# Kernel tuning notes

Measured on AMD Instinct MI355X. Metric: run time of the kernel, lower is better.

Reference implementation:

```python
import jax, jax.numpy as jnp
import numpy as np

B, S, D = 2, 2048, 1024
H, HD = 16, 64
HIDDEN = 2730  # int(1024 * 4 * 2/3)
WINDOW = 512
EPS = 1e-6


def rmsnorm(x, w):
    return x * jax.lax.rsqrt(jnp.mean(x * x, axis=-1, keepdims=True) + EPS) * w


def rope(q, k):
    # q, k: [B, H, S, HD]; half-split rotate_half convention, base 10000
    inv_freq = 1.0 / (10000.0 ** (jnp.arange(0, HD, 2, dtype=jnp.float32) / HD))
    pos = jnp.arange(S, dtype=jnp.float32)
    freqs = pos[:, None] * inv_freq[None, :]          # [S, HD/2]
    cos = jnp.concatenate([jnp.cos(freqs)] * 2, -1)    # [S, HD]
    sin = jnp.concatenate([jnp.sin(freqs)] * 2, -1)

    def rot_half(x):
        x1, x2 = jnp.split(x, 2, axis=-1)
        return jnp.concatenate([-x2, x1], axis=-1)

    q = q * cos + rot_half(q) * sin
    k = k * cos + rot_half(k) * sin
    return q, k


def setup_inputs() -> dict:
    key = jax.random.key(0)
    ks = jax.random.split(key, 6)
    return {
        "x": jax.random.normal(ks[0], (B, S, D), jnp.float32),
        "norm1_w": jnp.ones((D,), jnp.float32),
        "norm2_w": jnp.ones((D,), jnp.float32),
        "w_qkv": jax.random.normal(ks[1], (3 * D, D), jnp.float32) * 0.02,
        "qnorm_w": jnp.ones((HD,), jnp.float32),
        "knorm_w": jnp.ones((HD,), jnp.float32),
        "w_o": jax.random.normal(ks[2], (D, D), jnp.float32) * (0.02 / 2 ** 0.5),
        "w1": jax.random.normal(ks[3], (HIDDEN, D), jnp.float32) * 0.02,
        "w3": jax.random.normal(ks[4], (HIDDEN, D), jnp.float32) * 0.02,
        "w2": jax.random.normal(ks[5], (D, HIDDEN), jnp.float32) * 0.02,
    }


def reference(x, norm1_w, norm2_w, w_qkv, qnorm_w, knorm_w, w_o, w1, w3, w2):
    h = rmsnorm(x, norm1_w)                              # [B,S,D]
    qkv = jnp.einsum("bsd,ed->bse", h, w_qkv)            # [B,S,3D]
    q, k, v = jnp.split(qkv, 3, axis=-1)

    def heads(t):  # [B,S,D] -> [B,H,S,HD]
        return t.reshape(B, S, H, HD).transpose(0, 2, 1, 3)

    q, k, v = heads(q), heads(k), heads(v)
    q = rmsnorm(q, qnorm_w)  # qk_norm over head_dim
    k = rmsnorm(k, knorm_w)
    q, k = rope(q, k)

    scale = HD ** -0.5
    scores = jnp.einsum("bhqd,bhkd->bhqk", q, k) * scale  # [B,H,S,S]
    pos = jnp.arange(S)
    row, col = pos[:, None], pos[None, :]
    masked = (col > row) | (col < row - WINDOW + 1)       # True = don't attend
    scores = jnp.where(masked[None, None], -jnp.inf, scores)
    attn = jax.nn.softmax(scores, axis=-1)
    out = jnp.einsum("bhqk,bhkd->bhqd", attn, v)          # [B,H,S,HD]
    out = out.transpose(0, 2, 1, 3).reshape(B, S, D)
    out = jnp.einsum("bsd,ed->bse", out, w_o)

    x = x + out
    h2 = rmsnorm(x, norm2_w)
    gate = jax.nn.silu(jnp.einsum("bsd,hd->bsh", h2, w1))
    up = jnp.einsum("bsd,hd->bsh", h2, w3)
    ffn = jnp.einsum("bsh,dh->bsd", gate * up, w2)
    return x + ffn
```

## Files before the change

kernel.cpp:

```cpp
#include <hip/hip_runtime.h>

typedef unsigned short u16;
typedef unsigned int   u32;
typedef __bf16 bf16x8 __attribute__((ext_vector_type(8)));
typedef __bf16 bf16x2 __attribute__((ext_vector_type(2)));
typedef float  f32x4  __attribute__((ext_vector_type(4)));
typedef float  f32x2  __attribute__((ext_vector_type(2)));

#define DEV static __device__ __forceinline__
#define NEG_INF (-__builtin_inff())

DEV u16 f2bf(float f) {
  u32 u = __builtin_bit_cast(u32, f);
  u += 0x7fffu + ((u >> 16) & 1u);
  return (u16)(u >> 16);
}

DEV float bf2f(u16 v) {
  u32 u = (u32)v << 16;
  return __builtin_bit_cast(float, u);
}

DEV u32 packbf(float a, float b) {
  f32x2 v = {a, b};
  bf16x2 r = __builtin_convertvector(v, bf16x2);
  return __builtin_bit_cast(u32, r);
}

typedef __attribute__((address_space(1))) void gvoid_t;
typedef __attribute__((address_space(3))) void svoid_t;

DEV void async16(const void* g, void* l) {
  __builtin_amdgcn_global_load_lds((gvoid_t*)g, (svoid_t*)l, 16, 0, 0);
}

DEV f32x4 mfma_bf16(bf16x8 a, bf16x8 b, f32x4 c) {
  return __builtin_amdgcn_mfma_f32_16x16x32_bf16(a, b, c, 0, 0, 0);
}

#define SBAR() __builtin_amdgcn_sched_barrier(0)
#define BARRIER() do { SBAR(); __builtin_amdgcn_s_barrier(); SBAR(); } while (0)
#define LGK0() do { asm volatile("s_waitcnt lgkmcnt(0)" ::: "memory"); SBAR(); } while (0)
#define VMC(n) do { asm volatile("s_waitcnt vmcnt(" #n ")" ::: "memory"); SBAR(); } while (0)

__global__ void cvt_bf16_k(const float* __restrict__ s, u16* __restrict__ d, int n4) {
  int i = blockIdx.x * blockDim.x + threadIdx.x;
  if (i >= n4) return;
  float4 v = ((const float4*)s)[i];
  ((ushort4*)d)[i] = make_ushort4(f2bf(v.x), f2bf(v.y), f2bf(v.z), f2bf(v.w));
}

__global__ void w13_prep_k(const float* __restrict__ w1, const float* __restrict__ w3,
                           u16* __restrict__ d, int n4) {
  int i = blockIdx.x * blockDim.x + threadIdx.x;
  if (i >= n4) return;
  int e = i * 4;
  int r = e >> 10;
  int c = e & 1023;
  int blk = r >> 4, j = r & 15;
  int srow = (blk >> 1) * 16 + j;
  ushort4 o = make_ushort4(0, 0, 0, 0);
  if (srow < 2730) {
    const float* src = (blk & 1) ? w3 : w1;
    float4 v = *(const float4*)&src[(size_t)srow * 1024 + c];
    o = make_ushort4(f2bf(v.x), f2bf(v.y), f2bf(v.z), f2bf(v.w));
  }
  ((ushort4*)d)[i] = o;
}

__global__ void pad_cols_k(const float* __restrict__ s, u16* __restrict__ d,
                           int Cs, int Cd, int n4) {
  int i = blockIdx.x * blockDim.x + threadIdx.x;
  if (i >= n4) return;
  int e = i * 4;
  int r = e / Cd;
  int c = e - r * Cd;
  u16 o[4];
#pragma unroll
  for (int j = 0; j < 4; ++j) {
    int cc = c + j;
    o[j] = (cc < Cs) ? f2bf(s[(size_t)r * Cs + cc]) : (u16)0;
  }
  ((ushort4*)d)[i] = make_ushort4(o[0], o[1], o[2], o[3]);
}

__global__ void rmsnorm_cvt_k(const float* __restrict__ in, const float* __restrict__ w,
                              u16* __restrict__ out) {
  __shared__ float red[4];
  int row = blockIdx.x;
  int t = threadIdx.x;
  const float4 v = ((const float4*)(in + (size_t)row * 1024))[t];
  float ss = v.x * v.x + v.y * v.y + v.z * v.z + v.w * v.w;
#pragma unroll
  for (int off = 1; off < 64; off <<= 1) ss += __shfl_xor(ss, off);
  if ((t & 63) == 0) red[t >> 6] = ss;
  __syncthreads();
  float tot = red[0] + red[1] + red[2] + red[3];
  float rs = rsqrtf(tot * (1.0f / 1024.0f) + 1e-6f);
  const float4 wv = ((const float4*)w)[t];
  ((ushort4*)(out + (size_t)row * 1024))[t] =
      make_ushort4(f2bf(v.x * rs * wv.x), f2bf(v.y * rs * wv.y),
                   f2bf(v.z * rs * wv.z), f2bf(v.w * rs * wv.w));
}

__global__ void qk_post_k(const u16* __restrict__ qkv, const float* __restrict__ qw,
                          const float* __restrict__ kw, u16* __restrict__ Qb,
                          u16* __restrict__ Kb) {
  int g = blockIdx.x * 4 + (threadIdx.x >> 6);
  int d = threadIdx.x & 63;
  int b = g >> 15;
  int r = g & 32767;
  int s = r >> 4;
  int h = r & 15;
  size_t base = ((size_t)(b * 2048 + s)) * 3072 + h * 64 + d;
  float qv = bf2f(qkv[base]);
  float kv = bf2f(qkv[base + 1024]);
  float q2 = qv * qv, k2 = kv * kv;
#pragma unroll
  for (int off = 1; off < 64; off <<= 1) {
    q2 += __shfl_xor(q2, off);
    k2 += __shfl_xor(k2, off);
  }
  float qn = qv * rsqrtf(q2 * (1.0f / 64.0f) + 1e-6f) * qw[d];
  float kn = kv * rsqrtf(k2 * (1.0f / 64.0f) + 1e-6f) * kw[d];
  int j = d & 31;
  float invf = __expf((float)j * -0.28782313662425572f);
  float ang = (float)s * invf;
  float sn, cs;
  sincosf(ang, &sn, &cs);
  float pq = __shfl_xor(qn, 32);
  float pk = __shfl_xor(kn, 32);
  float qo = (d < 32) ? (qn * cs - pq * sn) : (qn * cs + pq * sn);
  float ko = (d < 32) ? (kn * cs - pk * sn) : (kn * cs + pk * sn);
  size_t ob = ((size_t)((b * 16 + h) * 2048 + s)) * 64 + d;
  Qb[ob] = f2bf(qo);
  Kb[ob] = f2bf(ko);
}

__global__ void vtrans_k(const u16* __restrict__ qkv, u16* __restrict__ VT) {
  __shared__ u16 tile[64][65];
  int bh = blockIdx.y;
  int b = bh >> 4, h = bh & 15;
  int s0 = blockIdx.x * 64;
  int t = threadIdx.x;
  int tx = t & 63, ty = t >> 6;
#pragma unroll
  for (int p = 0; p < 16; ++p) {
    int sl = p * 4 + ty;
    tile[sl][tx] = qkv[((size_t)(b * 2048 + s0 + sl)) * 3072 + 2048 + h * 64 + tx];
  }
  __syncthreads();
#pragma unroll
  for (int p = 0; p < 16; ++p) {
    int dl = p * 4 + ty;
    VT[((size_t)(bh * 64 + dl)) * 2048 + s0 + tx] = tile[tx][dl];
  }
}

template <int EPI>
__global__ __launch_bounds__(256, 1) void gemm128p(
    const u16* __restrict__ A, const u16* __restrict__ B0,
    const float* __restrict__ res, void* __restrict__ outp, int M, int N, int K, int NT) {
  __shared__ u16 S[49152];
  const int tid = threadIdx.x;
  const int lane = tid & 63;
  const int wv = tid >> 6;
  const int wr = wv >> 1;
  const int wc = wv & 1;
  const int c16 = lane & 15, g4 = lane >> 4;

  const int gx = gridDim.x;
  const int nwg = gx * gridDim.y;
  const int lin = blockIdx.x + gx * blockIdx.y;
  const int swz = (lin & 7) * (nwg >> 3) + (lin >> 3);
  const int bm = (swz / gx) * 128;
  const int bn = (swz % gx) * 128;

  const int strow = tid >> 3;
  const int stcs = ((tid & 7) ^ (strow & 7)) * 8;
  const u16* Ap = A + (size_t)(bm + strow) * K + stcs;
  const u16* Bp = B0 + (size_t)(bn + strow) * K + stcs;
  const int wvb = wv * 512;

#define STG(bufi, t) do { const size_t _o = (size_t)(t) * 64; _Pragma("unroll") \
    for (int s = 0; s < 4; ++s) { \
      async16(Ap + _o + (size_t)s * 32 * K, &S[(bufi) * 16384 + s * 2048 + wvb]); \
      async16(Bp + _o + (size_t)s * 32 * K, &S[(bufi) * 16384 + 8192 + s * 2048 + wvb]); \
    } } while (0)

  f32x4 acc[4][4] = {};
  const int xk0 = (g4 ^ (c16 & 7)) * 8;
  const int xk1 = ((4 + g4) ^ (c16 & 7)) * 8;
  const int arb = (wr * 64 + c16) * 64;
  const int brb = 8192 + (wc * 64 + c16) * 64;

  STG(0, 0);
  STG(1, 1);
  VMC(8); BARRIER();

  int cur = 0;
  for (int kt = 0; kt < NT; ++kt) {
    int n2 = cur + 2; if (n2 >= 3) n2 -= 3;
    if (kt + 2 < NT) {
      if (n2 == 0) STG(0, kt + 2);
      else if (n2 == 1) STG(1, kt + 2);
      else STG(2, kt + 2);
    }
    bf16x8 a[4][2], b[4][2];
    const int cb = cur * 16384;
#pragma unroll
    for (int mf = 0; mf < 4; ++mf) {
      a[mf][0] = *(const bf16x8*)&S[cb + arb + mf * 1024 + xk0];
      a[mf][1] = *(const bf16x8*)&S[cb + arb + mf * 1024 + xk1];
    }
#pragma unroll
    for (int nf = 0; nf < 4; ++nf) {
      b[nf][0] = *(const bf16x8*)&S[cb + brb + nf * 1024 + xk0];
      b[nf][1] = *(const bf16x8*)&S[cb + brb + nf * 1024 + xk1];
    }
    LGK0();
    __builtin_amdgcn_s_setprio(1);
#pragma unroll
    for (int ks = 0; ks < 2; ++ks)
#pragma unroll
      for (int mf = 0; mf < 4; ++mf)
#pragma unroll
        for (int nf = 0; nf < 4; ++nf)
          acc[mf][nf] = mfma_bf16(a[mf][ks], b[nf][ks], acc[mf][nf]);
    __builtin_amdgcn_s_setprio(0);
    if (kt + 2 < NT) { VMC(8); } else { VMC(0); }
    BARRIER();
    cur = cur + 1; if (cur >= 3) cur = 0;
  }

#pragma unroll
  for (int mf = 0; mf < 4; ++mf)
#pragma unroll
    for (int nf = 0; nf < 4; ++nf) {
      int row = bm + wr * 64 + mf * 16 + g4 * 4;
      int col = bn + wc * 64 + nf * 16 + c16;
#pragma unroll
      for (int r = 0; r < 4; ++r) {
        size_t idx = (size_t)(row + r) * (size_t)N + col;
        if constexpr (EPI == 1) {
          ((float*)outp)[idx] = res[idx] + acc[mf][nf][r];
        } else {
          ((u16*)outp)[idx] = f2bf(acc[mf][nf][r]);
        }
      }
    }
#undef STG
}

__global__ __launch_bounds__(512, 1) void gemm192(
    const u16* __restrict__ A, const u16* __restrict__ B0,
    u16* __restrict__ outp, int N, int K, int NT) {
  __shared__ u16 SA[32768];
  __shared__ u16 SB[24576];
  const int tid = threadIdx.x;
  const int lane = tid & 63;
  const int wv = tid >> 6;
  const int wr = wv >> 2;
  const int wc = wv & 3;
  const int c16 = lane & 15, g4 = lane >> 4;

  const int gx = gridDim.x;
  const int nwg = gx * gridDim.y;
  const int lin = blockIdx.x + gx * blockIdx.y;
  const int swz = (lin & 7) * (nwg >> 3) + (lin >> 3);
  const int bm = (swz / gx) * 256;
  const int bn = (swz % gx) * 192;

  const int sr = tid >> 2;
  const int sc2s = ((tid & 3) * 16) ^ (((sr >> 3) & 1) << 5);
  const int scol = sc2s >> 1;
  const u16* Asrc = A + (size_t)(bm + sr) * K + scol;
  const int ldst = wv * 512;
  const int brow = tid >> 3;
  const int bgr = (tid & 7) ^ (brow & 7);
  const u16* Bsrc = B0 + (size_t)(bn + brow) * K + bgr * 8;
  const int bldst = wv * 512;

#define STA_(buf, h, t) do { \
    const u16* _g = Asrc + (size_t)(h) * 128 * K + (t) * 64; \
    async16(_g,      &SA[(buf) * 16384 + (h) * 8192 + ldst]); \
    async16(_g + 32, &SA[(buf) * 16384 + (h) * 8192 + 4096 + ldst]); } while (0)
#define STB_(buf, p, t) do { \
    async16(Bsrc + (size_t)(p) * 64 * K + (t) * 64, \
            &SB[(buf) * 12288 + (p) * 4096 + bldst]); } while (0)

  const int xr = (g4 * 8) ^ (((c16 >> 3) & 1) << 4);
  const int raOff = c16 * 32 + xr;
  const int abase0 = wr * 8192;
  const int brow0 = wc * 48 + c16;
  const int bsw = c16 & 7;

#define LDA_(buf, qm) do { _Pragma("unroll") \
    for (int mf = 0; mf < 4; ++mf) { \
      int _ro = (buf) * 16384 + abase0 + ((qm) * 64 + mf * 16) * 32 + raOff; \
      a[mf][0] = *(const bf16x8*)&SA[_ro]; \
      a[mf][1] = *(const bf16x8*)&SA[_ro + 4096]; } } while (0)
#define LDB01_(buf) do { _Pragma("unroll") \
    for (int nf = 0; nf < 2; ++nf) { \
      int _r = (buf) * 12288 + (brow0 + nf * 16) * 64; \
      bq01[nf][0] = *(const bf16x8*)&SB[_r + ((g4) ^ bsw) * 8]; \
      bq01[nf][1] = *(const bf16x8*)&SB[_r + ((4 + g4) ^ bsw) * 8]; } } while (0)
#define LDB2_(buf) do { \
      int _r = (buf) * 12288 + (brow0 + 32) * 64; \
      bq2[0] = *(const bf16x8*)&SB[_r + ((g4) ^ bsw) * 8]; \
      bq2[1] = *(const bf16x8*)&SB[_r + ((4 + g4) ^ bsw) * 8]; } while (0)
#define MM16(qm) do { _Pragma("unroll") \
    for (int mf = 0; mf < 4; ++mf) _Pragma("unroll") \
      for (int nf = 0; nf < 2; ++nf) { \
        acc[(qm) * 4 + mf][nf] = mfma_bf16(a[mf][0], bq01[nf][0], acc[(qm) * 4 + mf][nf]); \
        acc[(qm) * 4 + mf][nf] = mfma_bf16(a[mf][1], bq01[nf][1], acc[(qm) * 4 + mf][nf]); } } while (0)
#define MM8(qm) do { _Pragma("unroll") \
    for (int mf = 0; mf < 4; ++mf) { \
      acc[(qm) * 4 + mf][2] = mfma_bf16(a[mf][0], bq2[0], acc[(qm) * 4 + mf][2]); \
      acc[(qm) * 4 + mf][2] = mfma_bf16(a[mf][1], bq2[1], acc[(qm) * 4 + mf][2]); } } while (0)

  f32x4 acc[8][3] = {};
  bf16x8 a[4][2], bq01[2][2], bq2[2];

  STB_(0, 0, 0); STB_(0, 1, 0); STB_(0, 2, 0); STA_(0, 0, 0); STA_(0, 1, 0);
  STB_(1, 0, 1); STB_(1, 1, 1); STB_(1, 2, 1); STA_(1, 0, 1); STA_(1, 1, 1);
  VMC(7); BARRIER();

  for (int kt = 0; kt < NT; ++kt) {
    const int buf = kt & 1;
    const int t2 = (kt + 2 < NT) ? kt + 2 : NT - 1;
    LDA_(buf, 0); LDB01_(buf);
    BARRIER(); LGK0();
    __builtin_amdgcn_s_setprio(1); MM16(0); __builtin_amdgcn_s_setprio(0);
    BARRIER();
    LDB2_(buf);
    BARRIER(); LGK0();
    __builtin_amdgcn_s_setprio(1); MM8(0); __builtin_amdgcn_s_setprio(0);
    BARRIER();
    LDA_(buf, 1);
    STB_(buf, 0, t2); STB_(buf, 1, t2); STB_(buf, 2, t2);
    BARRIER(); LGK0();
    __builtin_amdgcn_s_setprio(1); MM16(1); __builtin_amdgcn_s_setprio(0);
    BARRIER();
    STA_(buf, 0, t2); STA_(buf, 1, t2);
    BARRIER();
    __builtin_amdgcn_s_setprio(1); MM8(1); __builtin_amdgcn_s_setprio(0);
    VMC(7); BARRIER();
  }
  asm volatile("s_waitcnt vmcnt(0)" ::: "memory");

#pragma unroll
  for (int mf = 0; mf < 8; ++mf) {
    int row0 = bm + wr * 128 + mf * 16 + g4 * 4;
#pragma unroll
    for (int nf = 0; nf < 3; ++nf) {
      int col = bn + wc * 48 + nf * 16 + c16;
#pragma unroll
      for (int r = 0; r < 4; ++r)
        outp[(size_t)(row0 + r) * N + col] = f2bf(acc[mf][nf][r]);
    }
  }
#undef STA_
#undef STB_
#undef LDA_
#undef LDB01_
#undef LDB2_
#undef MM16
#undef MM8
}

template <int QM, int QN>
DEV void mmq(f32x4 (&acc)[8][4], const bf16x8 (&a)[4][2], const bf16x8 (&b)[2][2]) {
#pragma unroll
  for (int mf = 0; mf < 4; ++mf)
#pragma unroll
    for (int nf = 0; nf < 2; ++nf) {
      acc[QM * 4 + mf][QN * 2 + nf] = mfma_bf16(a[mf][0], b[nf][0], acc[QM * 4 + mf][QN * 2 + nf]);
      acc[QM * 4 + mf][QN * 2 + nf] = mfma_bf16(a[mf][1], b[nf][1], acc[QM * 4 + mf][QN * 2 + nf]);
    }
}

template <int EPI>
__global__ __launch_bounds__(512, 2) void gemm256(
    const u16* __restrict__ A, const u16* __restrict__ B0,
    void* __restrict__ outp, int M, int N, int K, int NT) {
  __shared__ u16 S[65536];
  const int tid = threadIdx.x;
  const int lane = tid & 63;
  const int wv = tid >> 6;
  const int wr = wv >> 2;
  const int wc = wv & 3;
  const int c16 = lane & 15, g4 = lane >> 4;

  int gx = gridDim.x;
  int nwg = gx * gridDim.y;
  int lin = blockIdx.x + gx * blockIdx.y;
  int swz = ((nwg & 7) == 0) ? ((lin & 7) * (nwg >> 3) + (lin >> 3)) : lin;
  const int bm = (swz / gx) * 256;
  const int bn = (swz % gx) * 256;

  const int sr = tid >> 2;
  const int sc2s = ((tid & 3) * 16) ^ (((sr >> 3) & 1) << 5);
  const int scol = sc2s >> 1;
  const u16* Asrc = A + (size_t)(bm + sr) * K + scol;
  const u16* Bsrc = B0 + (size_t)(bn + sr) * K + scol;
  const int ldst = wv * 512;

#define STA(buf, h, t) do { \
    const u16* _g = Asrc + (size_t)(h) * 128 * K + (t) * 64; \
    async16(_g,      &S[(buf) * 16384 + (h) * 8192 + ldst]); \
    async16(_g + 32, &S[(buf) * 16384 + (h) * 8192 + 4096 + ldst]); } while (0)
#define STB(buf, h, t) do { \
    const u16* _g = Bsrc + (size_t)(h) * 128 * K + (t) * 64; \
    async16(_g,      &S[32768 + (buf) * 16384 + (h) * 8192 + ldst]); \
    async16(_g + 32, &S[32768 + (buf) * 16384 + (h) * 8192 + 4096 + ldst]); } while (0)

  const int xr = (g4 * 8) ^ (((c16 >> 3) & 1) << 4);
  const int raOff = c16 * 32 + xr;
  const int abase0 = wr * 8192;
  const int bbase0 = 32768 + (wc >> 1) * 8192 + (wc & 1) * 2048;

#define LDA(buf, qm) do { _Pragma("unroll") \
    for (int mf = 0; mf < 4; ++mf) { \
      int _ro = (buf) * 16384 + abase0 + ((qm) * 64 + mf * 16) * 32 + raOff; \
      a[mf][0] = *(const bf16x8*)&S[_ro]; \
      a[mf][1] = *(const bf16x8*)&S[_ro + 4096]; } } while (0)
#define LDB(buf, qn, bq) do { _Pragma("unroll") \
    for (int nf = 0; nf < 2; ++nf) { \
      int _ro = (buf) * 16384 + bbase0 + ((qn) * 2 + nf) * 512 + raOff; \
      bq[nf][0] = *(const bf16x8*)&S[_ro]; \
      bq[nf][1] = *(const bf16x8*)&S[_ro + 4096]; } } while (0)

  f32x4 acc[8][4] = {};
  bf16x8 a[4][2], bq0[2][2], bq1[2][2];

  STB(0, 0, 0); STB(0, 1, 0); STA(0, 0, 0); STA(0, 1, 0);
  STB(1, 0, 1); STB(1, 1, 1); STA(1, 0, 1); STA(1, 1, 1);
  VMC(8); BARRIER();

  for (int kt = 0; kt < NT; ++kt) {
    const int buf = kt & 1;
    const int t2 = (kt + 2 < NT) ? kt + 2 : NT - 1;
    LDA(buf, 0); LDB(buf, 0, bq0);
    BARRIER(); LGK0();
    __builtin_amdgcn_s_setprio(1); mmq<0, 0>(acc, a, bq0); __builtin_amdgcn_s_setprio(0);
    BARRIER();
    LDB(buf, 1, bq1);
    BARRIER(); LGK0();
    __builtin_amdgcn_s_setprio(1); mmq<0, 1>(acc, a, bq1); __builtin_amdgcn_s_setprio(0);
    BARRIER();
    LDA(buf, 1);
    STB(buf, 0, t2); STB(buf, 1, t2);
    BARRIER(); LGK0();
    __builtin_amdgcn_s_setprio(1); mmq<1, 0>(acc, a, bq0); __builtin_amdgcn_s_setprio(0);
    BARRIER();
    STA(buf, 0, t2); STA(buf, 1, t2);
    BARRIER();
    __builtin_amdgcn_s_setprio(1); mmq<1, 1>(acc, a, bq1); __builtin_amdgcn_s_setprio(0);
    VMC(8); BARRIER();
  }
  asm volatile("s_waitcnt vmcnt(0)" ::: "memory");

#pragma unroll
  for (int mf = 0; mf < 8; ++mf) {
    int row0 = bm + wr * 128 + mf * 16 + g4 * 4;
    if constexpr (EPI == 0) {
#pragma unroll
      for (int nf = 0; nf < 4; ++nf) {
        int col = bn + wc * 64 + nf * 16 + c16;
#pragma unroll
        for (int r = 0; r < 4; ++r)
          ((float*)outp)[(size_t)(row0 + r) * N + col] = acc[mf][nf][r];
      }
    } else {
      const int NH = N >> 1;
#pragma unroll
      for (int p = 0; p < 2; ++p) {
        int hid = ((bn + wc * 64) >> 1) + p * 16 + c16;
#pragma unroll
        for (int r = 0; r < 4; ++r) {
          float gg = acc[mf][2 * p][r];
          float uu = acc[mf][2 * p + 1][r];
          ((u16*)outp)[(size_t)(row0 + r) * NH + hid] = f2bf(gg * uu / (1.0f + __expf(-gg)));
        }
      }
    }
  }
#undef STA
#undef STB
#undef LDA
#undef LDB
}

__global__ __launch_bounds__(256, 4) void attn_k(const u16* __restrict__ Q,
                                                 const u16* __restrict__ Kb,
                                                 const u16* __restrict__ VT,
                                                 u16* __restrict__ O) {
  __shared__ u16 KT[2 * 2048];
  __shared__ u16 VTl[2 * 2048];
  __shared__ float bsm[4][16];
  __shared__ u16 Plds[4][16 * 40];
  const int tid = threadIdx.x;
  const int lane = tid & 63;
  const int wv = tid >> 6;
  const int bh = blockIdx.y;
  const int q0b = blockIdx.x * 64;
  const int q0 = q0b + wv * 16;
  const int c16 = lane & 15;
  const int hi = lane >> 4;
  const u16* Qp = Q + ((size_t)bh * 2048 + q0) * 64;

  const bf16x8 qf0 = *(const bf16x8*)&Qp[c16 * 64 + hi * 8];
  const bf16x8 qf1 = *(const bf16x8*)&Qp[c16 * 64 + 32 + hi * 8];

  const int krow = tid >> 3;
  const int kcs = ((tid & 7) ^ (krow & 7)) * 8;
  const u16* Ksrc = Kb + (size_t)bh * 131072 + (size_t)krow * 64 + kcs;
  const int vrow = tid >> 2;
  const int vcs = ((tid & 3) ^ ((vrow >> 1) & 3)) * 8;
  const u16* Vsrc = VT + (size_t)bh * 131072 + (size_t)vrow * 2048 + vcs;
  const int wvb = wv * 512;

  f32x4 o[4] = {};
  float m = -30.0f;
  float psum = 0.0f;
  const float SCL = 0.125f * 1.4426950408889634f;
  int startb = q0b - 511;
  if (startb < 0) startb = 0;
  startb &= ~31;
  const int kgend = q0b + 32;
  u16* Pw = Plds[wv];
  float* bw = bsm[wv];

  const int xh0 = (hi ^ (c16 & 7)) * 8;
  const int xh4 = ((4 + hi) ^ (c16 & 7)) * 8;
  const int xv = (hi ^ ((c16 >> 1) & 3)) * 8;

  async16(Ksrc + (size_t)startb * 64, &KT[wvb]);
  async16(Vsrc + startb, &VTl[wvb]);

  int buf = 0;
  for (int kg = startb; kg <= kgend; kg += 32) {
    if (kg + 32 <= kgend) {
      async16(Ksrc + (size_t)(kg + 32) * 64, &KT[(buf ^ 1) * 2048 + wvb]);
      async16(Vsrc + (kg + 32), &VTl[(buf ^ 1) * 2048 + wvb]);
      VMC(2);
    } else {
      VMC(0);
    }
    BARRIER();
    if (kg <= q0 + 15 && kg >= q0 - 542) {
      const int kb = buf * 2048 + c16 * 64;
      bf16x8 k00 = *(const bf16x8*)&KT[kb + xh0];
      bf16x8 k01 = *(const bf16x8*)&KT[kb + xh4];
      bf16x8 k10 = *(const bf16x8*)&KT[kb + 1024 + xh0];
      bf16x8 k11 = *(const bf16x8*)&KT[kb + 1024 + xh4];
      bf16x8 vf[4];
#pragma unroll
      for (int n = 0; n < 4; ++n)
        vf[n] = *(const bf16x8*)&VTl[buf * 2048 + (n * 16 + c16) * 32 + xv];
      LGK0();

      f32x4 slo = {0.f, 0.f, 0.f, 0.f}, shi2 = {0.f, 0.f, 0.f, 0.f};
      __builtin_amdgcn_s_setprio(1);
      slo = mfma_bf16(k00, qf0, slo);
      slo = mfma_bf16(k01, qf1, slo);
      shi2 = mfma_bf16(k10, qf0, shi2);
      shi2 = mfma_bf16(k11, qf1, shi2);
      __builtin_amdgcn_s_setprio(0);

      float sc[8];
#pragma unroll
      for (int r = 0; r < 4; ++r) {
        sc[r] = slo[r] * SCL;
        sc[4 + r] = shi2[r] * SCL;
      }
      const bool inter = (kg + 31 <= q0) && (kg >= q0 - 496);
      if (!inter) {
        const int row = q0 + c16;
#pragma unroll
        for (int r = 0; r < 4; ++r) {
          int col = kg + hi * 4 + r;
          if (!(col <= row && col > row - 512)) sc[r] = -1e30f;
          int col2 = col + 16;
          if (!(col2 <= row && col2 > row - 512)) sc[4 + r] = -1e30f;
        }
      }
      float tmax = fmaxf(fmaxf(fmaxf(sc[0], sc[1]), fmaxf(sc[2], sc[3])),
                         fmaxf(fmaxf(sc[4], sc[5]), fmaxf(sc[6], sc[7])));
      tmax = fmaxf(tmax, __shfl_xor(tmax, 16));
      tmax = fmaxf(tmax, __shfl_xor(tmax, 32));
      if (__any(tmax > m + 8.0f)) {
        float mn = fmaxf(m, tmax);
        float corr = exp2f(m - mn);
        m = mn;
        psum *= corr;
        bw[c16] = corr;
        __builtin_amdgcn_wave_barrier();
        float cr[4];
#pragma unroll
        for (int r = 0; r < 4; ++r) cr[r] = bw[hi * 4 + r];
        __builtin_amdgcn_wave_barrier();
#pragma unroll
        for (int n = 0; n < 4; ++n)
#pragma unroll
          for (int r = 0; r < 4; ++r) o[n][r] *= cr[r];
      }
      float p[8];
#pragma unroll
      for (int i = 0; i < 8; ++i) p[i] = exp2f(sc[i] - m);
      psum += ((p[0] + p[1]) + (p[2] + p[3])) + ((p[4] + p[5]) + (p[6] + p[7]));

      uint2 wlo, whi2;
      wlo.x = packbf(p[0], p[1]);
      wlo.y = packbf(p[2], p[3]);
      whi2.x = packbf(p[4], p[5]);
      whi2.y = packbf(p[6], p[7]);
      *(uint2*)&Pw[c16 * 40 + hi * 4] = wlo;
      *(uint2*)&Pw[c16 * 40 + 16 + hi * 4] = whi2;
      __builtin_amdgcn_wave_barrier();
      bf16x8 pa = *(const bf16x8*)&Pw[c16 * 40 + hi * 8];
      __builtin_amdgcn_wave_barrier();
      __builtin_amdgcn_s_setprio(1);
#pragma unroll
      for (int n = 0; n < 4; ++n) o[n] = mfma_bf16(pa, vf[n], o[n]);
      __builtin_amdgcn_s_setprio(0);
    }
    BARRIER();
    buf ^= 1;
  }

  psum += __shfl_xor(psum, 16);
  psum += __shfl_xor(psum, 32);
  bw[c16] = psum;
  __builtin_amdgcn_wave_barrier();
  const int b = bh >> 4, h = bh & 15;
#pragma unroll
  for (int r = 0; r < 4; ++r) {
    float inv = 1.0f / bw[hi * 4 + r];
    int row = q0 + hi * 4 + r;
#pragma unroll
    for (int n = 0; n < 4; ++n)
      O[((size_t)(b * 2048 + row)) * 1024 + h * 64 + n * 16 + c16] = f2bf(o[n][r] * inv);
  }
}

extern "C" void kernel_launch(void* const* d_in, const int* in_sizes, int n_in,
                              void* d_out, int out_size, void* d_ws, size_t ws_size,
                              hipStream_t stream) {
  const float* x    = (const float*)d_in[0];
  const float* n1w  = (const float*)d_in[1];
  const float* n2w  = (const float*)d_in[2];
  const float* wqkv = (const float*)d_in[3];
  const float* qnw  = (const float*)d_in[4];
  const float* knw  = (const float*)d_in[5];
  const float* wo   = (const float*)d_in[6];
  const float* w1   = (const float*)d_in[7];
  const float* w3   = (const float*)d_in[8];
  const float* w2   = (const float*)d_in[9];
  float* out = (float*)d_out;
  char* ws = (char*)d_ws;

  u16*   wqkv_b = (u16*)(ws + 0);
  u16*   wo_b   = (u16*)(ws + 6291456);
  u16*   w13i   = (u16*)(ws + 8388608);
  u16*   w2p    = (u16*)(ws + 19922944);
  u16*   h_b    = (u16*)(ws + 25690112);
  u16*   qkv_b  = (u16*)(ws + 34078720);
  u16*   act_b  = (u16*)(ws + 34078720);
  u16*   Qb     = (u16*)(ws + 84410368);
  u16*   Kb     = (u16*)(ws + 92798976);
  u16*   VTb    = (u16*)(ws + 101187584);
  float* x2f    = (float*)(ws + 109576192);
  u16*   attn_b = h_b;
  u16*   h2_b   = Qb;

  cvt_bf16_k<<<3072, 256, 0, stream>>>(wqkv, wqkv_b, 786432);
  cvt_bf16_k<<<1024, 256, 0, stream>>>(wo, wo_b, 262144);
  w13_prep_k<<<5632, 256, 0, stream>>>(w1, w3, w13i, 1441792);
  pad_cols_k<<<2816, 256, 0, stream>>>(w2, w2p, 2730, 2816, 720896);

  rmsnorm_cvt_k<<<4096, 256, 0, stream>>>(x, n1w, h_b);
  gemm192<<<dim3(16, 16), 512, 0, stream>>>(h_b, wqkv_b, qkv_b, 3072, 1024, 16);
  qk_post_k<<<16384, 256, 0, stream>>>(qkv_b, qnw, knw, Qb, Kb);
  vtrans_k<<<dim3(32, 32), 256, 0, stream>>>(qkv_b, VTb);
  attn_k<<<dim3(32, 32), 256, 0, stream>>>(Qb, Kb, VTb, attn_b);
  gemm128p<1><<<dim3(8, 32), 256, 0, stream>>>(attn_b, wo_b, x, x2f, 4096, 1024, 1024, 16);
  rmsnorm_cvt_k<<<4096, 256, 0, stream>>>(x2f, n2w, h2_b);
  gemm256<3><<<dim3(22, 16), 512, 0, stream>>>(h2_b, w13i, act_b, 4096, 5632, 1024, 16);
  gemm128p<1><<<dim3(8, 32), 256, 0, stream>>>(act_b, w2p, x2f, out, 4096, 1024, 2816, 44);
}
```

Before: 233.9 us.

## Software-pipeline LDS fragment loads across iterations and cut barriers in GEMM loops

Restructures the main K-loop of both GEMM kernels so the next tile's A/B fragments are read from LDS during the tail MFMA phase of the current iteration. Partial lgkmcnt waits replace full waits plus barriers, reducing each iteration from many block barriers to two. The aim is to hide LDS read latency and barrier stalls behind MFMA work. The cost is more live registers, and correctness now depends on the wait counts and buffer reuse ordering being exactly right.

```diff
diff --git a/kernel.cpp b/kernel.cpp
--- a/kernel.cpp
+++ b/kernel.cpp
@@ -41,6 +41,7 @@
 #define SBAR() __builtin_amdgcn_sched_barrier(0)
 #define BARRIER() do { SBAR(); __builtin_amdgcn_s_barrier(); SBAR(); } while (0)
 #define LGK0() do { asm volatile("s_waitcnt lgkmcnt(0)" ::: "memory"); SBAR(); } while (0)
+#define LGKC(n) do { asm volatile("s_waitcnt lgkmcnt(" #n ")" ::: "memory"); SBAR(); } while (0)
 #define VMC(n) do { asm volatile("s_waitcnt vmcnt(" #n ")" ::: "memory"); SBAR(); } while (0)
 
 __global__ void cvt_bf16_k(const float* __restrict__ s, u16* __restrict__ d, int n4) {
@@ -325,29 +326,33 @@
   STB_(0, 0, 0); STB_(0, 1, 0); STB_(0, 2, 0); STA_(0, 0, 0); STA_(0, 1, 0);
   STB_(1, 0, 1); STB_(1, 1, 1); STB_(1, 2, 1); STA_(1, 0, 1); STA_(1, 1, 1);
   VMC(7); BARRIER();
+  LDA_(0, 0); LDB01_(0);
 
   for (int kt = 0; kt < NT; ++kt) {
-    const int buf = kt & 1;
+    const int buf = kt & 1, nbuf = buf ^ 1;
     const int t2 = (kt + 2 < NT) ? kt + 2 : NT - 1;
-    LDA_(buf, 0); LDB01_(buf);
-    BARRIER(); LGK0();
+    LDB2_(buf);
+    LGKC(2);
     __builtin_amdgcn_s_setprio(1); MM16(0); __builtin_amdgcn_s_setprio(0);
+    SBAR();
+    LGK0();
+    __builtin_amdgcn_s_setprio(1); MM8(0); __builtin_amdgcn_s_setprio(0);
+    SBAR();
+    LDA_(buf, 1);
+    LGK0();
     BARRIER();
-    LDB2_(buf);
-    BARRIER(); LGK0();
-    __builtin_amdgcn_s_setprio(1); MM8(0); __builtin_amdgcn_s_setprio(0);
+    STB_(buf, 0, t2); STB_(buf, 1, t2); STB_(buf, 2, t2);
+    STA_(buf, 0, t2); STA_(buf, 1, t2);
+    __builtin_amdgcn_s_setprio(1); MM16(1); __builtin_amdgcn_s_setprio(0);
+    SBAR();
+    VMC(7);
     BARRIER();
-    LDA_(buf, 1);
-    STB_(buf, 0, t2); STB_(buf, 1, t2); STB_(buf, 2, t2);
-    BARRIER(); LGK0();
-    __builtin_amdgcn_s_setprio(1); MM16(1); __builtin_amdgcn_s_setprio(0);
-    BARRIER();
-    STA_(buf, 0, t2); STA_(buf, 1, t2);
-    BARRIER();
+    LDB01_(nbuf);
     __builtin_amdgcn_s_setprio(1); MM8(1); __builtin_amdgcn_s_setprio(0);
-    VMC(7); BARRIER();
-  }
-  asm volatile("s_waitcnt vmcnt(0)" ::: "memory");
+    SBAR();
+    LDA_(nbuf, 0);
+  }
+  asm volatile("s_waitcnt vmcnt(0) lgkmcnt(0)" ::: "memory");
 
 #pragma unroll
   for (int mf = 0; mf < 8; ++mf) {
@@ -437,29 +442,33 @@
   STB(0, 0, 0); STB(0, 1, 0); STA(0, 0, 0); STA(0, 1, 0);
   STB(1, 0, 1); STB(1, 1, 1); STA(1, 0, 1); STA(1, 1, 1);
   VMC(8); BARRIER();
+  LDA(0, 0); LDB(0, 0, bq0);
 
   for (int kt = 0; kt < NT; ++kt) {
-    const int buf = kt & 1;
+    const int buf = kt & 1, nbuf = buf ^ 1;
     const int t2 = (kt + 2 < NT) ? kt + 2 : NT - 1;
-    LDA(buf, 0); LDB(buf, 0, bq0);
-    BARRIER(); LGK0();
+    LDB(buf, 1, bq1);
+    LGKC(4);
     __builtin_amdgcn_s_setprio(1); mmq<0, 0>(acc, a, bq0); __builtin_amdgcn_s_setprio(0);
+    SBAR();
+    LGK0();
+    __builtin_amdgcn_s_setprio(1); mmq<0, 1>(acc, a, bq1); __builtin_amdgcn_s_setprio(0);
+    SBAR();
+    LDA(buf, 1);
+    LGK0();
     BARRIER();
-    LDB(buf, 1, bq1);
-    BARRIER(); LGK0();
-    __builtin_amdgcn_s_setprio(1); mmq<0, 1>(acc, a, bq1); __builtin_amdgcn_s_setprio(0);
+    STB(buf, 0, t2); STB(buf, 1, t2);
+    STA(buf, 0, t2); STA(buf, 1, t2);
+    __builtin_amdgcn_s_setprio(1); mmq<1, 0>(acc, a, bq0); __builtin_amdgcn_s_setprio(0);
+    SBAR();
+    VMC(8);
     BARRIER();
-    LDA(buf, 1);
-    STB(buf, 0, t2); STB(buf, 1, t2);
-    BARRIER(); LGK0();
-    __builtin_amdgcn_s_setprio(1); mmq<1, 0>(acc, a, bq0); __builtin_amdgcn_s_setprio(0);
-    BARRIER();
-    STA(buf, 0, t2); STA(buf, 1, t2);
-    BARRIER();
+    LDB(nbuf, 0, bq0);
     __builtin_amdgcn_s_setprio(1); mmq<1, 1>(acc, a, bq1); __builtin_amdgcn_s_setprio(0);
-    VMC(8); BARRIER();
-  }
-  asm volatile("s_waitcnt vmcnt(0)" ::: "memory");
+    SBAR();
+    LDA(nbuf, 0);
+  }
+  asm volatile("s_waitcnt vmcnt(0) lgkmcnt(0)" ::: "memory");
 
 #pragma unroll
   for (int mf = 0; mf < 8; ++mf) {
```

After: 238.0 us. Within noise of the previous version (+1.8%).
